# Optimization experiments

Measured on AMD Instinct MI355X. Metric: run time of the kernel, lower is better.

## Reference

```python
import jax, jax.numpy as jnp
import numpy as np

B, L, H, NH = 2, 2048, 2048, 16
K = H // NH  # q/k head dim (num_slot) = 128
EPS = 1e-5
SCALE = K ** -0.5  # fla gla default scale = key_dim**-0.5


def setup_inputs() -> dict:
    key = jax.random.key(0)
    k0, k1, k2, k3, k4 = jax.random.split(key, 5)
    std = 0.02
    return {
        "hidden_states": jax.random.normal(k0, (B, L, H), dtype=jnp.float32),
        "Wq": jax.random.normal(k1, (K, H), dtype=jnp.float32) * std,
        "Wk": jax.random.normal(k2, (K, H), dtype=jnp.float32) * std,
        "Wog": jax.random.normal(k3, (H, H), dtype=jnp.float32) * std,
        "Wig": jax.random.normal(k4, (H, H), dtype=jnp.float32) * std,
        "g_weight": jnp.ones((H,), dtype=jnp.float32),
    }


def _gla(q, k, v, g):
    # q,k: [B,L,K]; v: [B,L,V]; g: [B,L,K] (log decay per key dim)
    # recurrence: S_t = exp(g_t)[:, :, None] * S_{t-1} + k_t^T v_t ; o_t = q_t @ S_t
    def step(S, xs):
        q_t, k_t, v_t, g_t = xs  # [B,K],[B,K],[B,V],[B,K]
        S = jnp.exp(g_t)[:, :, None] * S + k_t[:, :, None] * v_t[:, None, :]
        o_t = jnp.einsum('bk,bkv->bv', q_t, S)
        return S, o_t

    S0 = jnp.zeros((q.shape[0], q.shape[2], v.shape[2]), dtype=q.dtype)
    xs = (jnp.swapaxes(q, 0, 1), jnp.swapaxes(k, 0, 1),
          jnp.swapaxes(v, 0, 1), jnp.swapaxes(g, 0, 1))
    _, o = jax.lax.scan(step, S0, xs)  # o: [L,B,V]
    return jnp.swapaxes(o, 0, 1)


def reference(hidden_states, Wq, Wk, Wog, Wig, g_weight):
    x = hidden_states
    q = x @ Wq.T  # [B,L,K]
    k_sig = jax.nn.sigmoid(x @ Wk.T)  # k = sigmoid(k_proj(x))
    q = jax.nn.silu(q) * SCALE  # swish feature map on q; fold in GLA scale
    gf = jax.nn.log_sigmoid(-k_sig)  # per-key log decay gates
    o = _gla(q, k_sig, x, gf)  # [B,L,H] (single head, V = hidden)
    # output gate + fused RMSNorm-SwishGate
    go = o @ Wog.T + x @ Wig.T
    rms = o * jax.lax.rsqrt(jnp.mean(o * o, axis=-1, keepdims=True) + EPS) * g_weight
    return rms * go * jax.nn.sigmoid(go)
```

## Files before the change

### kernel.cpp

```cpp
#include <hip/hip_runtime.h>
#include <math.h>

#define B_ 2
#define L_ 2048
#define H_ 2048
#define KD_ 128
#define SCALE_ 0.08838834764831845f
#define EPS_ 1e-5f
#define K2_ 4096

typedef __bf16 bf16x8 __attribute__((ext_vector_type(8)));
typedef float f32x4 __attribute__((ext_vector_type(4)));

static __device__ __forceinline__ float sigmoidf_(float z) {
    return 1.0f / (1.0f + __expf(-z));
}

static __device__ __forceinline__ unsigned short f2bf(float f) {
    unsigned int u = __float_as_uint(f);
    unsigned int r = (u + 0x7fffu + ((u >> 16) & 1u)) >> 16;
    return (unsigned short)r;
}

static __device__ __forceinline__ float bf2f(unsigned short s) {
    return __uint_as_float(((unsigned int)s) << 16);
}

#define ASYNC_COPY16(gsrc, ldst)                                             \
    __builtin_amdgcn_global_load_lds(                                        \
        (const __attribute__((address_space(1))) unsigned int*)(gsrc),       \
        (__attribute__((address_space(3))) unsigned int*)(ldst), 16, 0, 0)

#define BAR()                                                                \
    do {                                                                     \
        asm volatile("" ::: "memory");                                       \
        __builtin_amdgcn_s_barrier();                                        \
        asm volatile("" ::: "memory");                                       \
    } while (0)

#define JOBA_BLKS 4096
#define JOBB_BLKS 256
#define JOBC_BLKS 4096

__global__ __launch_bounds__(256) void prep_all(
    const float* __restrict__ x, const float* __restrict__ Wq,
    const float* __restrict__ Wk, const float* __restrict__ Wog,
    const float* __restrict__ Wig, unsigned short* __restrict__ Abuf,
    unsigned short* __restrict__ Wqk, unsigned short* __restrict__ Bbuf,
    float* __restrict__ rrms_acc)
{
    const int blk = blockIdx.x;
    const float* src;
    unsigned short* dst;
    if (blk < JOBA_BLKS) {
        size_t i = (size_t)blk * 256 + threadIdx.x;
        size_t m = i >> 8, c8 = (i & 255) * 8;
        src = x + m * H_ + c8;
        dst = Abuf + m * K2_ + H_ + c8;
    } else if (blk < JOBA_BLKS + JOBB_BLKS) {
        size_t i = (size_t)(blk - JOBA_BLKS) * 256 + threadIdx.x;
        if (i < 4096) rrms_acc[i] = 0.f;
        const size_t half = (size_t)KD_ * H_ / 8;
        src = ((i < half) ? Wq : Wk) + ((i < half) ? i : i - half) * 8;
        dst = Wqk + i * 8;
    } else {
        size_t i = (size_t)(blk - JOBA_BLKS - JOBB_BLKS) * 256 + threadIdx.x;
        const size_t half = (size_t)H_ * H_ / 8;
        size_t j = (i < half) ? i : i - half;
        size_t n = j >> 8, c8 = (j & 255) * 8;
        src = ((i < half) ? Wog : Wig) + n * H_ + c8;
        dst = Bbuf + n * K2_ + ((i < half) ? 0 : H_) + c8;
    }
    float4 v0 = *(const float4*)src;
    float4 v1 = *(const float4*)(src + 4);
    ushort4 a, b;
    a.x = f2bf(v0.x); a.y = f2bf(v0.y); a.z = f2bf(v0.z); a.w = f2bf(v0.w);
    b.x = f2bf(v1.x); b.y = f2bf(v1.y); b.z = f2bf(v1.z); b.w = f2bf(v1.w);
    *(ushort4*)dst = a;
    *(ushort4*)(dst + 4) = b;
}

__global__ __launch_bounds__(256) void qk_proj_mfma(
    const unsigned short* __restrict__ Abuf,
    const unsigned short* __restrict__ Wqk,
    float* __restrict__ partial)
{
    __shared__ alignas(16) unsigned short As[128 * 64];
    __shared__ alignas(16) unsigned short Bs[128 * 64];
    const int tid  = threadIdx.x;
    const int wave = tid >> 6;
    const int lane = tid & 63;
    const int m0 = blockIdx.x * 128;
    const int n0 = blockIdx.y * 128;
    const int kz = blockIdx.z * 512;
    const int wm = (wave >> 1) * 64;
    const int wn = (wave & 1) * 64;

    f32x4 acc[4][4] = {};

    const int se  = lane * 8;
    const int ldsbase = (wave * 4) * 512;
    const int frow = lane & 15;
    const int fk   = (lane >> 4) * 8;
    const int gswz = (((lane & 7) ^ (lane >> 3)) << 3);
    const int rswz = ((lane & 7) << 3);

    for (int k0 = kz; k0 < kz + 512; k0 += 64) {
        #pragma unroll
        for (int it = 0; it < 4; ++it) {
            int e = ldsbase + it * 512 + se;
            int r = e >> 6;
            const unsigned short* ga =
                Abuf + (size_t)(m0 + r) * K2_ + H_ + k0 + gswz;
            ASYNC_COPY16(ga, &As[e]);
            const unsigned short* gb = Wqk + (size_t)(n0 + r) * H_ + k0 + gswz;
            ASYNC_COPY16(gb, &Bs[e]);
        }
        __syncthreads();
        #pragma unroll
        for (int ksub = 0; ksub < 2; ++ksub) {
            bf16x8 af[4], bf[4];
            #pragma unroll
            for (int i = 0; i < 4; ++i)
                af[i] = *(const bf16x8*)(As + (wm + i * 16 + frow) * 64 +
                                         ((ksub * 32 + fk) ^ rswz));
            #pragma unroll
            for (int j = 0; j < 4; ++j)
                bf[j] = *(const bf16x8*)(Bs + (wn + j * 16 + frow) * 64 +
                                         ((ksub * 32 + fk) ^ rswz));
            #pragma unroll
            for (int i = 0; i < 4; ++i)
                #pragma unroll
                for (int j = 0; j < 4; ++j)
                    acc[i][j] = __builtin_amdgcn_mfma_f32_16x16x32_bf16(
                        af[i], bf[j], acc[i][j], 0, 0, 0);
        }
        __syncthreads();
    }

    float* pz = partial + (size_t)blockIdx.z * 4096 * 256;
    #pragma unroll
    for (int i = 0; i < 4; ++i) {
        #pragma unroll
        for (int reg = 0; reg < 4; ++reg) {
            int m = m0 + wm + i * 16 + (lane >> 4) * 4 + reg;
            #pragma unroll
            for (int j = 0; j < 4; ++j) {
                int n = n0 + wn + j * 16 + (lane & 15);
                pz[(size_t)m * 256 + n] = acc[i][j][reg];
            }
        }
    }
}

__global__ __launch_bounds__(256) void scan_scale_kernel(
    const float* __restrict__ partial,
    unsigned short* __restrict__ qt_b, unsigned short* __restrict__ kA_b,
    unsigned short* __restrict__ kB_b)
{
    const int c = blockIdx.x, b = blockIdx.y;
    const int kd = blockIdx.z * 32 + (threadIdx.x & 31);
    const int rg = threadIdx.x >> 5;
    const size_t stride = (size_t)4096 * 256;
    const int row0 = b * L_ + c * 64 + rg * 8;

    float qv[8], kv[8], gp[8];
    float run = 0.f;
    #pragma unroll
    for (int j = 0; j < 8; ++j) {
        size_t off = (size_t)(row0 + j) * 256;
        float sq = partial[off + kd] + partial[stride + off + kd]
                 + partial[2 * stride + off + kd] + partial[3 * stride + off + kd];
        float sk = partial[off + 128 + kd] + partial[stride + off + 128 + kd]
                 + partial[2 * stride + off + 128 + kd]
                 + partial[3 * stride + off + 128 + kd];
        float ksv = sigmoidf_(sk);
        qv[j] = sq * sigmoidf_(sq) * SCALE_;
        kv[j] = ksv;
        run += -log1pf(__expf(ksv));
        gp[j] = run;
    }
    __shared__ float s_seg[8][32];
    s_seg[rg][threadIdx.x & 31] = run;
    __syncthreads();
    float base = 0.f, total = 0.f;
    #pragma unroll
    for (int r = 0; r < 8; ++r) {
        float v = s_seg[r][threadIdx.x & 31];
        base += (r < rg) ? v : 0.f;
        total += v;
    }
    #pragma unroll
    for (int j = 0; j < 8; ++j) {
        float s = base + gp[j];
        size_t idx = (size_t)(row0 + j) * KD_ + kd;
        qt_b[idx] = f2bf(qv[j] * __expf(s));
        kA_b[idx] = f2bf(kv[j] * __expf(-s));
        kB_b[idx] = f2bf(kv[j] * __expf(total - s));
    }
}

__global__ __launch_bounds__(256) void p_kernel(
    const unsigned short* __restrict__ qt_b,
    const unsigned short* __restrict__ kA_b,
    const unsigned short* __restrict__ kB_b,
    unsigned short* __restrict__ Pbuf)
{
    const int c = blockIdx.x, b = blockIdx.y;
    const int tid = threadIdx.x;
    const int w = tid >> 6, l = tid & 63;
    const int lr = l & 15, lq = l >> 4;
    const int q0 = c * 64;
    const size_t rowbase = (size_t)b * L_;

    bf16x8 aq[4];
    {
        const unsigned short* qrow = qt_b + (rowbase + q0 + 16 * w + lr) * KD_;
        #pragma unroll
        for (int kt = 0; kt < 4; ++kt)
            aq[kt] = *(const bf16x8*)(qrow + kt * 32 + lq * 8);
    }
    unsigned short* pout = Pbuf + (size_t)(b * 32 + c) * 64 * 128;
    #pragma unroll
    for (int jt = 0; jt < 8; ++jt) {
        f32x4 p = {};
        const int si = jt * 16 + lr;
        const bool prev = (jt < 4);
        const bool dead = (c == 0 && prev);
        if (!dead) {
            int kp = prev ? (q0 - 64 + si) : (q0 + si - 64);
            const unsigned short* kb = (prev ? kB_b : kA_b) + (rowbase + kp) * KD_;
            #pragma unroll
            for (int kt = 0; kt < 4; ++kt) {
                bf16x8 bk = *(const bf16x8*)(kb + kt * 32 + lq * 8);
                p = __builtin_amdgcn_mfma_f32_16x16x32_bf16(aq[kt], bk, p, 0, 0, 0);
            }
        }
        #pragma unroll
        for (int reg = 0; reg < 4; ++reg) {
            int ti = 16 * w + lq * 4 + reg;
            bool keep = !dead && (si <= ti + 64);
            pout[ti * 128 + si] = keep ? f2bf(p[reg]) : (unsigned short)0;
        }
    }
}

#define SV_ 130

__global__ __launch_bounds__(256) void pv_kernel(
    const unsigned short* __restrict__ Pbuf,
    unsigned short* Abuf,
    float* __restrict__ rrms_acc)
{
    const int c  = blockIdx.x;
    const int b  = blockIdx.y;
    const int vt = blockIdx.z;
    const int tid = threadIdx.x;
    const int w = tid >> 6, l = tid & 63;
    const int lr = l & 15, lq = l >> 4;
    const int q0 = c * 64, kpos0 = q0 - 64, v0c = vt * 128;
    const size_t rowbase = (size_t)b * L_;

    __shared__ alignas(16) unsigned short Vt[128 * SV_];

    {
        const int a = tid & 15;
        const int kr0 = tid >> 4;
        for (int kr = kr0; kr < 128; kr += 16) {
            int kp = kpos0 + kr;
            ushort4 u0 = {0, 0, 0, 0}, u1 = {0, 0, 0, 0};
            if (kp >= 0) {
                const unsigned short* src =
                    Abuf + (rowbase + kp) * K2_ + H_ + v0c + a * 8;
                u0 = *(const ushort4*)src;
                u1 = *(const ushort4*)(src + 4);
            }
            unsigned short vals[8] = {u0.x, u0.y, u0.z, u0.w,
                                      u1.x, u1.y, u1.z, u1.w};
            #pragma unroll
            for (int j = 0; j < 8; ++j)
                Vt[(a * 8 + j) * SV_ + kr] = vals[j];
        }
    }

    bf16x8 ap[4];
    {
        const unsigned short* prow =
            Pbuf + ((size_t)(b * 32 + c) * 64 + 16 * w + lr) * 128;
        #pragma unroll
        for (int kt = 0; kt < 4; ++kt)
            ap[kt] = *(const bf16x8*)(prow + kt * 32 + lq * 8);
    }
    __syncthreads();

    float rsum[4] = {0.f, 0.f, 0.f, 0.f};
    #pragma unroll
    for (int jt = 0; jt < 8; ++jt) {
        f32x4 oa = {};
        const int n = jt * 16 + lr;
        #pragma unroll
        for (int kt = 0; kt < 4; ++kt) {
            const unsigned int* vp =
                (const unsigned int*)(Vt + n * SV_ + kt * 32 + lq * 8);
            union { unsigned int u[4]; bf16x8 v; } bb;
            bb.u[0] = vp[0]; bb.u[1] = vp[1]; bb.u[2] = vp[2]; bb.u[3] = vp[3];
            oa = __builtin_amdgcn_mfma_f32_16x16x32_bf16(ap[kt], bb.v, oa, 0, 0, 0);
        }
        #pragma unroll
        for (int reg = 0; reg < 4; ++reg) {
            int qrow = 16 * w + lq * 4 + reg;
            size_t orow = rowbase + q0 + qrow;
            float val = oa[reg];
            Abuf[orow * K2_ + v0c + n] = f2bf(val);
            rsum[reg] += val * val;
        }
    }
    #pragma unroll
    for (int mk = 1; mk < 16; mk <<= 1) {
        #pragma unroll
        for (int reg = 0; reg < 4; ++reg)
            rsum[reg] += __shfl_xor(rsum[reg], mk, 64);
    }
    if (lr == 0) {
        #pragma unroll
        for (int reg = 0; reg < 4; ++reg)
            atomicAdd(&rrms_acc[rowbase + q0 + 16 * w + lq * 4 + reg], rsum[reg]);
    }
}

__global__ __launch_bounds__(512, 2) void out_gemm_mfma(
    const unsigned short* __restrict__ Abuf,
    const unsigned short* __restrict__ Bbuf,
    const float* __restrict__ gw, const float* __restrict__ rrms_acc,
    float* __restrict__ out)
{
    __shared__ alignas(16) unsigned short As[3 * 256 * 64];
    __shared__ alignas(16) unsigned short Bs[3 * 128 * 64];
    const int tid  = threadIdx.x;
    const int w    = tid >> 6;
    const int lane = tid & 63;
    const int wr   = w >> 1;
    const int wc   = w & 1;
    const int m0 = blockIdx.x * 256;
    const int n0 = blockIdx.y * 128;

    const int frow = lane & 15;
    const int fkb  = (lane >> 4) << 3;
    const int rxor = (lane & 7) << 3;

    const int srow = tid >> 3;
    const int scol = (((tid & 7) ^ (srow & 7)) << 3);
    const unsigned short* agsrc = Abuf + (size_t)(m0 + srow) * K2_ + scol;
    const unsigned short* bgsrc = Bbuf + (size_t)(n0 + srow) * K2_ + scol;
    unsigned short* As_dst = As + tid * 8;
    unsigned short* Bs_dst = Bs + tid * 8;

#define STAGE_A_(cb, k0)                                                     \
    {                                                                        \
        _Pragma("unroll")                                                    \
        for (int it_ = 0; it_ < 4; ++it_)                                    \
            ASYNC_COPY16(agsrc + (size_t)(it_ * 64) * K2_ + (k0),            \
                         As_dst + (cb) * 16384 + it_ * 4096);                \
    }
#define STAGE_B_(cb, k0)                                                     \
    {                                                                        \
        _Pragma("unroll")                                                    \
        for (int it_ = 0; it_ < 2; ++it_)                                    \
            ASYNC_COPY16(bgsrc + (size_t)(it_ * 64) * K2_ + (k0),            \
                         Bs_dst + (cb) * 8192 + it_ * 4096);                 \
    }
#define LDA_(buf, i_, ks_)                                                   \
    (*(const bf16x8*)((buf) + (wr * 64 + (i_) * 16 + frow) * 64 +            \
                      (((ks_) * 32 + fkb) ^ rxor)))
#define LDB_(buf, j_, ks_)                                                   \
    (*(const bf16x8*)((buf) + (wc * 64 + (j_) * 16 + frow) * 64 +            \
                      (((ks_) * 32 + fkb) ^ rxor)))
#define MFMA_(a_, b_, c_)                                                    \
    (c_) = __builtin_amdgcn_mfma_f32_16x16x32_bf16((a_), (b_), (c_), 0, 0, 0)

    f32x4 acc[4][4] = {};

    STAGE_A_(0, 0); STAGE_B_(0, 0);
    STAGE_A_(1, 64); STAGE_B_(1, 64);
    asm volatile("s_waitcnt vmcnt(6)" ::: "memory");
    BAR();

    int cur = 0;
    for (int t = 0; t < 64; ++t) {
        const unsigned short* Ab = As + cur * 16384;
        const unsigned short* Bb = Bs + cur * 8192;
        int stg = cur + 2; if (stg >= 3) stg -= 3;
        const int kpre = (t + 2) * 64;
        const bool pre = (t + 2 < 64);
        bf16x8 af[2][2], bfr[4][2];

        #pragma unroll
        for (int ii = 0; ii < 2; ++ii) {
            af[ii][0] = LDA_(Ab, ii, 0);
            af[ii][1] = LDA_(Ab, ii, 1);
        }
        #pragma unroll
        for (int j = 0; j < 2; ++j) {
            bfr[j][0] = LDB_(Bb, j, 0);
            bfr[j][1] = LDB_(Bb, j, 1);
        }
        if (pre) STAGE_A_(stg, kpre);
        BAR();
        __builtin_amdgcn_s_setprio(1);
        #pragma unroll
        for (int ii = 0; ii < 2; ++ii)
            #pragma unroll
            for (int j = 0; j < 2; ++j) {
                MFMA_(af[ii][0], bfr[j][0], acc[ii][j]);
                MFMA_(af[ii][1], bfr[j][1], acc[ii][j]);
            }
        __builtin_amdgcn_s_setprio(0);
        BAR();

        #pragma unroll
        for (int j = 0; j < 2; ++j) {
            bfr[2 + j][0] = LDB_(Bb, 2 + j, 0);
            bfr[2 + j][1] = LDB_(Bb, 2 + j, 1);
        }
        if (pre) STAGE_B_(stg, kpre);
        BAR();
        __builtin_amdgcn_s_setprio(1);
        #pragma unroll
        for (int ii = 0; ii < 2; ++ii)
            #pragma unroll
            for (int j = 0; j < 2; ++j) {
                MFMA_(af[ii][0], bfr[2 + j][0], acc[ii][2 + j]);
                MFMA_(af[ii][1], bfr[2 + j][1], acc[ii][2 + j]);
            }
        __builtin_amdgcn_s_setprio(0);
        BAR();

        #pragma unroll
        for (int ii = 0; ii < 2; ++ii) {
            af[ii][0] = LDA_(Ab, 2 + ii, 0);
            af[ii][1] = LDA_(Ab, 2 + ii, 1);
        }
        BAR();
        __builtin_amdgcn_s_setprio(1);
        #pragma unroll
        for (int ii = 0; ii < 2; ++ii)
            #pragma unroll
            for (int j = 0; j < 2; ++j) {
                MFMA_(af[ii][0], bfr[j][0], acc[2 + ii][j]);
                MFMA_(af[ii][1], bfr[j][1], acc[2 + ii][j]);
            }
        __builtin_amdgcn_s_setprio(0);
        BAR();

        __builtin_amdgcn_s_setprio(1);
        #pragma unroll
        for (int ii = 0; ii < 2; ++ii)
            #pragma unroll
            for (int j = 0; j < 2; ++j) {
                MFMA_(af[ii][0], bfr[2 + j][0], acc[2 + ii][2 + j]);
                MFMA_(af[ii][1], bfr[2 + j][1], acc[2 + ii][2 + j]);
            }
        __builtin_amdgcn_s_setprio(0);
        if (pre) { asm volatile("s_waitcnt vmcnt(6)" ::: "memory"); }
        else     { asm volatile("s_waitcnt vmcnt(0)" ::: "memory"); }
        BAR();
        cur = cur + 1; if (cur == 3) cur = 0;
    }

#undef STAGE_A_
#undef STAGE_B_
#undef LDA_
#undef LDB_
#undef MFMA_

    #pragma unroll
    for (int i = 0; i < 4; ++i) {
        #pragma unroll
        for (int reg = 0; reg < 4; ++reg) {
            int m = m0 + wr * 64 + i * 16 + (lane >> 4) * 4 + reg;
            float rv = rsqrtf(rrms_acc[m] * (1.0f / H_) + EPS_);
            #pragma unroll
            for (int j = 0; j < 4; ++j) {
                int n = n0 + wc * 64 + j * 16 + (lane & 15);
                float go = acc[i][j][reg];
                float ov = bf2f(Abuf[(size_t)m * K2_ + n]);
                out[(size_t)m * H_ + n] = ov * rv * gw[n] * go * sigmoidf_(go);
            }
        }
    }
}

extern "C" void kernel_launch(void* const* d_in, const int* in_sizes, int n_in,
                              void* d_out, int out_size, void* d_ws, size_t ws_size,
                              hipStream_t stream) {
    (void)in_sizes; (void)n_in; (void)out_size; (void)ws_size;
    const float* x   = (const float*)d_in[0];
    const float* Wq  = (const float*)d_in[1];
    const float* Wk  = (const float*)d_in[2];
    const float* Wog = (const float*)d_in[3];
    const float* Wig = (const float*)d_in[4];
    const float* gw  = (const float*)d_in[5];
    float* out = (float*)d_out;

    const size_t MK = (size_t)B_ * L_ * KD_;
    unsigned short* Abuf = (unsigned short*)d_ws;
    unsigned short* Bbuf = Abuf + (size_t)4096 * K2_;
    unsigned short* qt_b = Bbuf + (size_t)2048 * K2_;
    unsigned short* kA_b = qt_b + MK;
    unsigned short* kB_b = kA_b + MK;
    unsigned short* Wqk  = kB_b + MK;
    unsigned short* Pbuf = Wqk + (size_t)256 * H_;
    float* partial  = (float*)(Pbuf + (size_t)64 * 64 * 128);
    float* rrms_acc = partial + (size_t)4 * 4096 * 256;

    prep_all<<<JOBA_BLKS + JOBB_BLKS + JOBC_BLKS, 256, 0, stream>>>(
        x, Wq, Wk, Wog, Wig, Abuf, Wqk, Bbuf, rrms_acc);
    qk_proj_mfma<<<dim3(32, 2, 4), 256, 0, stream>>>(Abuf, Wqk, partial);
    scan_scale_kernel<<<dim3(32, B_, 4), 256, 0, stream>>>(partial, qt_b, kA_b, kB_b);
    p_kernel<<<dim3(32, B_), 256, 0, stream>>>(qt_b, kA_b, kB_b, Pbuf);
    pv_kernel<<<dim3(32, B_, 16), 256, 0, stream>>>(Pbuf, Abuf, rrms_acc);
    out_gemm_mfma<<<dim3(16, 16), 512, 0, stream>>>(Abuf, Bbuf, gw, rrms_acc, out);
}
```

Before: 265.0 us.

## Reshape output GEMM tile to 128x256 with 2x4 warps and two-phase schedule

```diff
diff --git a/kernel.cpp b/kernel.cpp
--- a/kernel.cpp
+++ b/kernel.cpp
@@ -334,15 +334,16 @@
     const float* __restrict__ gw, const float* __restrict__ rrms_acc,
     float* __restrict__ out)
 {
-    __shared__ alignas(16) unsigned short As[3 * 256 * 64];
-    __shared__ alignas(16) unsigned short Bs[3 * 128 * 64];
+    __shared__ alignas(16) unsigned short As[3 * 128 * 64];
+    __shared__ alignas(16) unsigned short Bs[3 * 256 * 64];
     const int tid  = threadIdx.x;
+    const int lane = tid & 63;
     const int w    = tid >> 6;
-    const int lane = tid & 63;
-    const int wr   = w >> 1;
-    const int wc   = w & 1;
-    const int m0 = blockIdx.x * 256;
-    const int n0 = blockIdx.y * 128;
+    const int wrow = w >> 2;
+    const int wcol = w & 3;
+    const int bid  = blockIdx.x;
+    const int m0 = (bid >> 3) * 128;
+    const int n0 = (bid & 7) * 256;
 
     const int frow = lane & 15;
     const int fkb  = (lane >> 4) << 3;
@@ -355,120 +356,86 @@
     unsigned short* As_dst = As + tid * 8;
     unsigned short* Bs_dst = Bs + tid * 8;
 
-#define STAGE_A_(cb, k0)                                                     \
+#define STAGE_A2_(cb, k0)                                                    \
     {                                                                        \
-        _Pragma("unroll")                                                    \
-        for (int it_ = 0; it_ < 4; ++it_)                                    \
-            ASYNC_COPY16(agsrc + (size_t)(it_ * 64) * K2_ + (k0),            \
-                         As_dst + (cb) * 16384 + it_ * 4096);                \
-    }
-#define STAGE_B_(cb, k0)                                                     \
-    {                                                                        \
-        _Pragma("unroll")                                                    \
-        for (int it_ = 0; it_ < 2; ++it_)                                    \
-            ASYNC_COPY16(bgsrc + (size_t)(it_ * 64) * K2_ + (k0),            \
-                         Bs_dst + (cb) * 8192 + it_ * 4096);                 \
-    }
+        ASYNC_COPY16(agsrc + (k0), As_dst + (cb) * 8192);                    \
+        ASYNC_COPY16(agsrc + (size_t)64 * K2_ + (k0),                        \
+                     As_dst + (cb) * 8192 + 4096);                           \
+    }
+#define STAGE_B1_(cb, k0, it_)                                               \
+    ASYNC_COPY16(bgsrc + (size_t)((it_) * 64) * K2_ + (k0),                  \
+                 Bs_dst + (cb) * 16384 + (it_) * 4096)
 #define LDA_(buf, i_, ks_)                                                   \
-    (*(const bf16x8*)((buf) + (wr * 64 + (i_) * 16 + frow) * 64 +            \
+    (*(const bf16x8*)(As + (buf) * 8192 +                                    \
+                      (wrow * 64 + (i_) * 16 + frow) * 64 +                  \
                       (((ks_) * 32 + fkb) ^ rxor)))
 #define LDB_(buf, j_, ks_)                                                   \
-    (*(const bf16x8*)((buf) + (wc * 64 + (j_) * 16 + frow) * 64 +            \
+    (*(const bf16x8*)(Bs + (buf) * 16384 +                                   \
+                      (wcol * 64 + (j_) * 16 + frow) * 64 +                  \
                       (((ks_) * 32 + fkb) ^ rxor)))
 #define MFMA_(a_, b_, c_)                                                    \
     (c_) = __builtin_amdgcn_mfma_f32_16x16x32_bf16((a_), (b_), (c_), 0, 0, 0)
 
     f32x4 acc[4][4] = {};
 
-    STAGE_A_(0, 0); STAGE_B_(0, 0);
-    STAGE_A_(1, 64); STAGE_B_(1, 64);
+    STAGE_A2_(0, 0);
+    STAGE_B1_(0, 0, 0); STAGE_B1_(0, 0, 1); STAGE_B1_(0, 0, 2); STAGE_B1_(0, 0, 3);
+    STAGE_A2_(1, 64);
+    STAGE_B1_(1, 64, 0); STAGE_B1_(1, 64, 1); STAGE_B1_(1, 64, 2); STAGE_B1_(1, 64, 3);
     asm volatile("s_waitcnt vmcnt(6)" ::: "memory");
     BAR();
 
     int cur = 0;
     for (int t = 0; t < 64; ++t) {
-        const unsigned short* Ab = As + cur * 16384;
-        const unsigned short* Bb = Bs + cur * 8192;
         int stg = cur + 2; if (stg >= 3) stg -= 3;
         const int kpre = (t + 2) * 64;
         const bool pre = (t + 2 < 64);
-        bf16x8 af[2][2], bfr[4][2];
-
-        #pragma unroll
-        for (int ii = 0; ii < 2; ++ii) {
-            af[ii][0] = LDA_(Ab, ii, 0);
-            af[ii][1] = LDA_(Ab, ii, 1);
-        }
-        #pragma unroll
-        for (int j = 0; j < 2; ++j) {
-            bfr[j][0] = LDB_(Bb, j, 0);
-            bfr[j][1] = LDB_(Bb, j, 1);
-        }
-        if (pre) STAGE_A_(stg, kpre);
+        bf16x8 af[4], bfr[4];
+
+        #pragma unroll
+        for (int i = 0; i < 4; ++i) af[i] = LDA_(cur, i, 0);
+        #pragma unroll
+        for (int j = 0; j < 4; ++j) bfr[j] = LDB_(cur, j, 0);
+        if (pre) {
+            STAGE_A2_(stg, kpre);
+            STAGE_B1_(stg, kpre, 0);
+        }
         BAR();
         __builtin_amdgcn_s_setprio(1);
         #pragma unroll
-        for (int ii = 0; ii < 2; ++ii)
-            #pragma unroll
-            for (int j = 0; j < 2; ++j) {
-                MFMA_(af[ii][0], bfr[j][0], acc[ii][j]);
-                MFMA_(af[ii][1], bfr[j][1], acc[ii][j]);
-            }
+        for (int i = 0; i < 4; ++i)
+            #pragma unroll
+            for (int j = 0; j < 4; ++j)
+                MFMA_(af[i], bfr[j], acc[i][j]);
         __builtin_amdgcn_s_setprio(0);
         BAR();
 
         #pragma unroll
-        for (int j = 0; j < 2; ++j) {
-            bfr[2 + j][0] = LDB_(Bb, 2 + j, 0);
-            bfr[2 + j][1] = LDB_(Bb, 2 + j, 1);
-        }
-        if (pre) STAGE_B_(stg, kpre);
-        BAR();
-        __builtin_amdgcn_s_setprio(1);
-        #pragma unroll
-        for (int ii = 0; ii < 2; ++ii)
-            #pragma unroll
-            for (int j = 0; j < 2; ++j) {
-                MFMA_(af[ii][0], bfr[2 + j][0], acc[ii][2 + j]);
-                MFMA_(af[ii][1], bfr[2 + j][1], acc[ii][2 + j]);
-            }
-        __builtin_amdgcn_s_setprio(0);
-        BAR();
-
-        #pragma unroll
-        for (int ii = 0; ii < 2; ++ii) {
-            af[ii][0] = LDA_(Ab, 2 + ii, 0);
-            af[ii][1] = LDA_(Ab, 2 + ii, 1);
-        }
-        BAR();
-        __builtin_amdgcn_s_setprio(1);
-        #pragma unroll
-        for (int ii = 0; ii < 2; ++ii)
-            #pragma unroll
-            for (int j = 0; j < 2; ++j) {
-                MFMA_(af[ii][0], bfr[j][0], acc[2 + ii][j]);
-                MFMA_(af[ii][1], bfr[j][1], acc[2 + ii][j]);
-            }
-        __builtin_amdgcn_s_setprio(0);
-        BAR();
-
-        __builtin_amdgcn_s_setprio(1);
-        #pragma unroll
-        for (int ii = 0; ii < 2; ++ii)
-            #pragma unroll
-            for (int j = 0; j < 2; ++j) {
-                MFMA_(af[ii][0], bfr[2 + j][0], acc[2 + ii][2 + j]);
-                MFMA_(af[ii][1], bfr[2 + j][1], acc[2 + ii][2 + j]);
-            }
-        __builtin_amdgcn_s_setprio(0);
+        for (int i = 0; i < 4; ++i) af[i] = LDA_(cur, i, 1);
+        #pragma unroll
+        for (int j = 0; j < 4; ++j) bfr[j] = LDB_(cur, j, 1);
+        if (pre) {
+            STAGE_B1_(stg, kpre, 1);
+            STAGE_B1_(stg, kpre, 2);
+            STAGE_B1_(stg, kpre, 3);
+        }
         if (pre) { asm volatile("s_waitcnt vmcnt(6)" ::: "memory"); }
         else     { asm volatile("s_waitcnt vmcnt(0)" ::: "memory"); }
         BAR();
+        __builtin_amdgcn_s_setprio(1);
+        #pragma unroll
+        for (int i = 0; i < 4; ++i)
+            #pragma unroll
+            for (int j = 0; j < 4; ++j)
+                MFMA_(af[i], bfr[j], acc[i][j]);
+        __builtin_amdgcn_s_setprio(0);
+        BAR();
+
         cur = cur + 1; if (cur == 3) cur = 0;
     }
 
-#undef STAGE_A_
-#undef STAGE_B_
+#undef STAGE_A2_
+#undef STAGE_B1_
 #undef LDA_
 #undef LDB_
 #undef MFMA_
@@ -477,11 +444,11 @@
     for (int i = 0; i < 4; ++i) {
         #pragma unroll
         for (int reg = 0; reg < 4; ++reg) {
-            int m = m0 + wr * 64 + i * 16 + (lane >> 4) * 4 + reg;
+            int m = m0 + wrow * 64 + i * 16 + (lane >> 4) * 4 + reg;
             float rv = rsqrtf(rrms_acc[m] * (1.0f / H_) + EPS_);
             #pragma unroll
             for (int j = 0; j < 4; ++j) {
-                int n = n0 + wc * 64 + j * 16 + (lane & 15);
+                int n = n0 + wcol * 64 + j * 16 + (lane & 15);
                 float go = acc[i][j][reg];
                 float ov = bf2f(Abuf[(size_t)m * K2_ + n]);
                 out[(size_t)m * H_ + n] = ov * rv * gw[n] * go * sigmoidf_(go);
@@ -519,5 +486,5 @@
     scan_scale_kernel<<<dim3(32, B_, 4), 256, 0, stream>>>(partial, qt_b, kA_b, kB_b);
     p_kernel<<<dim3(32, B_), 256, 0, stream>>>(qt_b, kA_b, kB_b, Pbuf);
     pv_kernel<<<dim3(32, B_, 16), 256, 0, stream>>>(Pbuf, Abuf, rrms_acc);
-    out_gemm_mfma<<<dim3(16, 16), 512, 0, stream>>>(Abuf, Bbuf, gw, rrms_acc, out);
-}
+    out_gemm_mfma<<<256, 512, 0, stream>>>(Abuf, Bbuf, gw, rrms_acc, out);
+}
```

After: 242.2 us. 1.09x faster.
